# Optimization experiments

Measured on AMD Instinct MI355X. Metric: run time of the kernel, lower is better.

Reference implementation:

```python
import jax, jax.numpy as jnp
import numpy as np

N_LAYERS = 2
D_MODEL = 768
D_INNER = 1536
D_STATE = 16
D_CONV = 4
DT_RANK = 48
VOCAB = 50257
EPS = 1e-5


def _rms(x, w):
    return x * jax.lax.rsqrt(jnp.mean(x * x, axis=-1, keepdims=True) + EPS) * w


def _mixer(x, in_w, cw, cb, xp_w, dt_w, dt_b, a_log, d_skip, out_w):
    b, l, _ = x.shape
    xz = x @ in_w.T                                  # (b,l,2*d_in)
    u, z = jnp.split(xz, 2, axis=-1)                 # each (b,l,d_in)
    # causal depthwise conv1d
    uc = jax.lax.conv_general_dilated(
        u.transpose(0, 2, 1), cw[:, None, :], (1,), [(D_CONV - 1, 0)],
        feature_group_count=D_INNER, dimension_numbers=("NCH", "OIH", "NCH"))
    u = jax.nn.silu((uc + cb[:, None]).transpose(0, 2, 1))
    x_dbl = u @ xp_w.T                               # (b,l,dt_rank+2n)
    dt, B, C = jnp.split(x_dbl, [DT_RANK, DT_RANK + D_STATE], axis=-1)
    delta = jax.nn.softplus(dt @ dt_w.T + dt_b)      # (b,l,d_in)
    A = -jnp.exp(a_log)                              # (d_in,n)
    dA = jnp.exp(delta[..., None] * A)               # (b,l,d_in,n)
    dBu = delta[..., None] * B[:, :, None, :] * u[..., None]

    def step(h, inp):
        dA_t, dBu_t, C_t = inp
        h = dA_t * h + dBu_t
        return h, jnp.einsum("bdn,bn->bd", h, C_t)

    h0 = jnp.zeros((b, D_INNER, D_STATE), x.dtype)
    _, ys = jax.lax.scan(step, h0, (dA.transpose(1, 0, 2, 3),
                                    dBu.transpose(1, 0, 2, 3),
                                    C.transpose(1, 0, 2)))
    y = ys.transpose(1, 0, 2) + u * d_skip           # (b,l,d_in)
    y = y * jax.nn.silu(z)
    return y @ out_w.T


def setup_inputs() -> dict:
    key = jax.random.key(0)
    ks = jax.random.split(key, 12)
    std = 0.02
    emb = jax.random.normal(ks[0], (VOCAB, D_MODEL), jnp.float32) * std
    emb = emb.at[0].set(0.0)  # padding_idx=0
    tokens = jax.random.randint(ks[1], (2, 1024), 0, VOCAB)
    a_log = jnp.tile(jnp.log(jnp.arange(1, D_STATE + 1, dtype=jnp.float32)),
                     (N_LAYERS, D_INNER, 1))
    return {
        "tokens": tokens,
        "emb": emb,
        "norm_w": jnp.ones((N_LAYERS, D_MODEL), jnp.float32),
        "in_proj_w": jax.random.normal(ks[2], (N_LAYERS, 2 * D_INNER, D_MODEL), jnp.float32) * std,
        "conv_w": jax.random.normal(ks[3], (N_LAYERS, D_INNER, D_CONV), jnp.float32) * 0.1,
        "conv_b": jnp.zeros((N_LAYERS, D_INNER), jnp.float32),
        "x_proj_w": jax.random.normal(ks[4], (N_LAYERS, DT_RANK + 2 * D_STATE, D_INNER), jnp.float32) * std,
        "dt_proj_w": jax.random.normal(ks[5], (N_LAYERS, D_INNER, DT_RANK), jnp.float32) * (DT_RANK ** -0.5),
        "dt_proj_b": jax.random.uniform(ks[6], (N_LAYERS, D_INNER), jnp.float32, -4.6, -2.0),
        "A_log": a_log,
        "D": jnp.ones((N_LAYERS, D_INNER), jnp.float32),
        "out_proj_w": jax.random.normal(ks[7], (N_LAYERS, D_MODEL, D_INNER), jnp.float32) * (std / np.sqrt(2 * N_LAYERS)),
        "normf_w": jnp.ones((D_MODEL,), jnp.float32),
        "lm_head_w": jax.random.normal(ks[8], (VOCAB, D_MODEL), jnp.float32) * std,
    }


def reference(tokens, emb, norm_w, in_proj_w, conv_w, conv_b, x_proj_w,
              dt_proj_w, dt_proj_b, A_log, D, out_proj_w, normf_w, lm_head_w):
    x = emb[tokens]                                  # (b,l,d_model)
    for i in range(N_LAYERS):
        x = x + _mixer(_rms(x, norm_w[i]), in_proj_w[i], conv_w[i], conv_b[i],
                       x_proj_w[i], dt_proj_w[i], dt_proj_b[i], A_log[i],
                       D[i], out_proj_w[i])
    x = _rms(x, normf_w)
    return x @ lm_head_w.T                           # (b,l,vocab)
```

## Files before the change

kernel.cpp:

```cpp
#include <hip/hip_runtime.h>
#include <hip/hip_bf16.h>
#include <math.h>

#define DM 768
#define DI 1536
#define DSN 16
#define NB 2
#define SL 1024
#define MROWS 2048
#define VOC 50257
#define VOCP 50432
#define EPSR 1e-5f

typedef __attribute__((ext_vector_type(8))) short short8;
typedef __attribute__((ext_vector_type(4))) float f32x4;
typedef __attribute__((ext_vector_type(4))) unsigned short us4;
typedef unsigned short u16;

__device__ inline u16 f2bf(float f) {
    unsigned u = __builtin_bit_cast(unsigned, f);
    u += 0x7FFFu + ((u >> 16) & 1u);
    return (u16)(u >> 16);
}

#define G_LDS16(g, l) __builtin_amdgcn_global_load_lds( \
    (const __attribute__((address_space(1))) void*)(g), \
    (__attribute__((address_space(3))) void*)(l), 16, 0, 0)

__global__ __launch_bounds__(256)
void k_embed_rms(const int* __restrict__ tok, const float* __restrict__ emb,
                 const float* __restrict__ w, float* __restrict__ x,
                 u16* __restrict__ out) {
    int r = blockIdx.x;
    int t = tok[r];
    const float* src = emb + (size_t)t * DM;
    int c0 = threadIdx.x * 3;
    float v[3]; float ss = 0.f;
#pragma unroll
    for (int i = 0; i < 3; ++i) {
        v[i] = src[c0 + i]; ss += v[i] * v[i];
        x[(size_t)r * DM + c0 + i] = v[i];
    }
#pragma unroll
    for (int o = 32; o > 0; o >>= 1) ss += __shfl_down(ss, o);
    __shared__ float s[4];
    int lane = threadIdx.x & 63, wv = threadIdx.x >> 6;
    if (lane == 0) s[wv] = ss;
    __syncthreads();
    float sc = rsqrtf((s[0] + s[1] + s[2] + s[3]) / (float)DM + EPSR);
#pragma unroll
    for (int i = 0; i < 3; ++i)
        out[(size_t)r * DM + c0 + i] = f2bf(v[i] * sc * w[c0 + i]);
}

__global__ __launch_bounds__(256)
void k_rmsnorm_bf16(const float* __restrict__ x, const float* __restrict__ w,
                    u16* __restrict__ out) {
    int r = blockIdx.x;
    const float* row = x + (size_t)r * DM;
    int c0 = threadIdx.x * 3;
    float v[3]; float ss = 0.f;
#pragma unroll
    for (int i = 0; i < 3; ++i) { v[i] = row[c0 + i]; ss += v[i] * v[i]; }
#pragma unroll
    for (int o = 32; o > 0; o >>= 1) ss += __shfl_down(ss, o);
    __shared__ float s[4];
    int lane = threadIdx.x & 63, wv = threadIdx.x >> 6;
    if (lane == 0) s[wv] = ss;
    __syncthreads();
    float sc = rsqrtf((s[0] + s[1] + s[2] + s[3]) / (float)DM + EPSR);
#pragma unroll
    for (int i = 0; i < 3; ++i)
        out[(size_t)r * DM + c0 + i] = f2bf(v[i] * sc * w[c0 + i]);
}

struct CvtSeg { const float* src; u16* dst; int sr, sc, sld, dc, blk0, total4; };
struct CvtArgs { CvtSeg seg[9]; };

__global__ __launch_bounds__(256)
void k_cvt_multi(CvtArgs a) {
    int b = blockIdx.x;
    int s = 0;
#pragma unroll
    for (int q = 1; q < 9; ++q) if (a.seg[q].blk0 <= b) s = q;
    const CvtSeg& g = a.seg[s];
    long i4 = (long)(b - g.blk0) * 256 + threadIdx.x;
    if (i4 >= g.total4) return;
    long i = i4 * 4;
    int r = (int)(i / g.dc), c0 = (int)(i % g.dc);
    us4 o;
#pragma unroll
    for (int e = 0; e < 4; ++e) {
        int c = c0 + e;
        float v = (r < g.sr && c < g.sc) ? g.src[(size_t)r * g.sld + c] : 0.f;
        o[e] = f2bf(v);
    }
    *(us4*)&g.dst[i] = o;
}

__global__ void k_conv_silu(const float* __restrict__ xz, const float* __restrict__ cw,
                            const float* __restrict__ cb, float* __restrict__ uc,
                            u16* __restrict__ ucb) {
    int d = blockIdx.x * 256 + threadIdx.x;
    int r = blockIdx.y;
    int l = r & (SL - 1);
    float acc = cb[d];
#pragma unroll
    for (int j = 0; j < 4; ++j) {
        int ls = l - 3 + j;
        if (ls >= 0) acc += xz[(size_t)(r - 3 + j) * (2 * DI) + d] * cw[d * 4 + j];
    }
    float s = acc / (1.f + __expf(-acc));
    uc[(size_t)r * DI + d] = s;
    ucb[(size_t)r * DI + d] = f2bf(s);
}

__global__ __launch_bounds__(256)
void k_xp_red(const float* __restrict__ part, float* __restrict__ xdbl,
              u16* __restrict__ xdblb) {
    int idx = blockIdx.x * 256 + threadIdx.x;
    int row = idx >> 7, col = idx & 127;
    const float* p = part + (size_t)row * 1024 + col;
    float s = 0.f;
#pragma unroll
    for (int k = 0; k < 8; ++k) s += p[k * 128];
    xdbl[(size_t)row * 128 + col] = s;
    if (col < 64) xdblb[(size_t)row * 64 + col] = f2bf(s);
}

__global__ __launch_bounds__(512)
void k_scan2(const float* __restrict__ delta, const float* __restrict__ uc,
             const float* __restrict__ xdbl, const float* __restrict__ xz,
             const float* __restrict__ alog, const float* __restrict__ Dp,
             u16* __restrict__ ybf) {
    __shared__ float ds2[8][16][20], us2[8][16][20], bn2[8][16][20], cn2[8][16][20];
    __shared__ float Sm[8][16][16], Pm[8][16][16];
    int b  = blockIdx.x / 96;
    int d0 = (blockIdx.x % 96) * 16;
    int tid = threadIdx.x, w = tid >> 6, lane = tid & 63;
    int ch = lane >> 2, nq = lane & 3;
    int d = d0 + ch;
    float A[4];
#pragma unroll
    for (int k = 0; k < 4; ++k) A[k] = -__expf(alog[d * DSN + nq + 4 * k]);
    int tb = w * 128;

    float h[4] = {0.f, 0.f, 0.f, 0.f};
    float sdl = 0.f;
    for (int t0 = 0; t0 < 128; t0 += 16) {
        int row0 = b * SL + tb + t0;
#pragma unroll
        for (int i = 0; i < 4; ++i) {
            int lin = i * 64 + lane, tt = lin >> 4, cc = lin & 15;
            size_t row = (size_t)(row0 + tt);
            ds2[w][cc][tt] = delta[row * DI + d0 + cc];
            us2[w][cc][tt] = uc[row * DI + d0 + cc];
            bn2[w][cc][tt] = xdbl[row * 128 + 48 + cc];
        }
#pragma unroll
        for (int g4 = 0; g4 < 4; ++g4) {
            f32x4 dl = *(const f32x4*)&ds2[w][ch][g4 * 4];
            f32x4 uv = *(const f32x4*)&us2[w][ch][g4 * 4];
            f32x4 bv[4];
#pragma unroll
            for (int k = 0; k < 4; ++k) bv[k] = *(const f32x4*)&bn2[w][nq + 4 * k][g4 * 4];
#pragma unroll
            for (int s = 0; s < 4; ++s) {
                float du = dl[s] * uv[s];
                sdl += dl[s];
#pragma unroll
                for (int k = 0; k < 4; ++k) {
                    float dA = __expf(dl[s] * A[k]);
                    h[k] = h[k] * dA + du * bv[k][s];
                }
            }
        }
    }
#pragma unroll
    for (int k = 0; k < 4; ++k) {
        Sm[w][ch][nq + 4 * k] = h[k];
        Pm[w][ch][nq + 4 * k] = __expf(A[k] * sdl);
    }
    __syncthreads();
    if (tid < 256) {
        int c2 = tid >> 4, n2 = tid & 15;
        float H = 0.f;
#pragma unroll
        for (int g = 0; g < 8; ++g) {
            float hi = H;
            H = Pm[g][c2][n2] * H + Sm[g][c2][n2];
            Sm[g][c2][n2] = hi;
        }
    }
    __syncthreads();
    float Dv = Dp[d];
#pragma unroll
    for (int k = 0; k < 4; ++k) h[k] = Sm[w][ch][nq + 4 * k];
    for (int t0 = 0; t0 < 128; t0 += 16) {
        int row0 = b * SL + tb + t0;
#pragma unroll
        for (int i = 0; i < 4; ++i) {
            int lin = i * 64 + lane, tt = lin >> 4, cc = lin & 15;
            size_t row = (size_t)(row0 + tt);
            ds2[w][cc][tt] = delta[row * DI + d0 + cc];
            us2[w][cc][tt] = uc[row * DI + d0 + cc];
            bn2[w][cc][tt] = xdbl[row * 128 + 48 + cc];
            cn2[w][cc][tt] = xdbl[row * 128 + 64 + cc];
        }
#pragma unroll
        for (int g4 = 0; g4 < 4; ++g4) {
            f32x4 dl = *(const f32x4*)&ds2[w][ch][g4 * 4];
            f32x4 uv = *(const f32x4*)&us2[w][ch][g4 * 4];
            f32x4 bv[4], cv[4];
#pragma unroll
            for (int k = 0; k < 4; ++k) {
                bv[k] = *(const f32x4*)&bn2[w][nq + 4 * k][g4 * 4];
                cv[k] = *(const f32x4*)&cn2[w][nq + 4 * k][g4 * 4];
            }
#pragma unroll
            for (int s = 0; s < 4; ++s) {
                float du = dl[s] * uv[s];
                float p = 0.f;
#pragma unroll
                for (int k = 0; k < 4; ++k) {
                    float dA = __expf(dl[s] * A[k]);
                    h[k] = h[k] * dA + du * bv[k][s];
                    p += h[k] * cv[k][s];
                }
                p += __shfl_xor(p, 1);
                p += __shfl_xor(p, 2);
                if (nq == 0) {
                    size_t row = (size_t)(row0 + g4 * 4 + s);
                    float z = xz[row * (2 * DI) + DI + d];
                    float y = p + uv[s] * Dv;
                    y *= z / (1.f + __expf(-z));
                    ybf[row * DI + d] = f2bf(y);
                }
            }
        }
    }
}

template <int EPIL, bool SPLITK>
__global__ __launch_bounds__(256)
void k_gemm_bt(const u16* __restrict__ A, const u16* __restrict__ W,
               float* C, const float* RES,
               const float* __restrict__ BIASV,
               int K, int ldk, int ldc, int nTm) {
    __shared__ u16 Al[128 * 32];
    __shared__ u16 Wl[128 * 32];
    int nwg = gridDim.x;
    int qc = nwg >> 3, rc = nwg & 7;
    int xcd = blockIdx.x & 7, j = blockIdx.x >> 3;
    int wg = (xcd < rc ? xcd * (qc + 1) : rc * (qc + 1) + (xcd - rc) * qc) + j;
    int m0 = (wg % nTm) * 128;
    int sl = wg / nTm;
    int n0 = SPLITK ? 0 : sl * 128;
    int cb = SPLITK ? sl * 128 : n0;
    int kb = SPLITK ? sl * K : 0;

    int tid = threadIdx.x, wave = tid >> 6, lane = tid & 63;
    int wm = wave >> 1, wn = wave & 1;
    f32x4 acc[4][4] = {};
    const int rS = (lane >> 2);
    const int kS = (((lane & 3) ^ ((lane >> 3) & 3)) * 8);
    const int kofs = (((lane >> 4) ^ ((lane >> 1) & 3)) * 8);
    const int fr = lane & 15;

    for (int k0 = 0; k0 < K; k0 += 32) {
#pragma unroll
        for (int i = 0; i < 2; ++i) {
            int rowA = m0 + wave * 32 + i * 16 + rS;
            G_LDS16(A + (size_t)rowA * ldk + kb + k0 + kS, &Al[wave * 1024 + i * 512]);
            int rowW = n0 + wave * 32 + i * 16 + rS;
            G_LDS16(W + (size_t)rowW * ldk + kb + k0 + kS, &Wl[wave * 1024 + i * 512]);
        }
        __syncthreads();
        short8 af[4], bfr[4];
#pragma unroll
        for (int f = 0; f < 4; ++f) {
            af[f]  = *(const short8*)&Al[(wm * 64 + f * 16 + fr) * 32 + kofs];
            bfr[f] = *(const short8*)&Wl[(wn * 64 + f * 16 + fr) * 32 + kofs];
        }
#pragma unroll
        for (int i = 0; i < 4; ++i)
#pragma unroll
            for (int jj = 0; jj < 4; ++jj)
                acc[i][jj] = __builtin_amdgcn_mfma_f32_16x16x32_bf16(af[i], bfr[jj], acc[i][jj], 0, 0, 0);
        __syncthreads();
    }
    int r4 = (lane >> 4) * 4;
#pragma unroll
    for (int i = 0; i < 4; ++i)
#pragma unroll
        for (int jj = 0; jj < 4; ++jj) {
            int col = cb + wn * 64 + jj * 16 + fr;
            float bia = (EPIL == 2) ? BIASV[col] : 0.f;
#pragma unroll
            for (int rr = 0; rr < 4; ++rr) {
                int row = m0 + wm * 64 + i * 16 + r4 + rr;
                size_t off = (size_t)row * ldc + col;
                float v = acc[i][jj][rr];
                if (EPIL == 1) v += RES[off];
                if (EPIL == 2) { v += bia; v = (v > 20.f) ? v : log1pf(__expf(v)); }
                C[off] = v;
            }
        }
}

#define BAR  __builtin_amdgcn_s_barrier()
#define LGK0 do { asm volatile("s_waitcnt lgkmcnt(0)" ::: "memory"); \
                  __builtin_amdgcn_sched_barrier(0); } while (0)
#define VMC3 asm volatile("s_waitcnt vmcnt(3)" ::: "memory")
#define VMC0 asm volatile("s_waitcnt vmcnt(0)" ::: "memory")

#define STAGE1(t, op, half, GB, RB) do {                                      \
    const u16* _g = (GB) + (size_t)((RB) + (half) * 128 + (w << 4) + srow) * K \
                    + (t) * 32 + scol;                                         \
    G_LDS16(_g, &lds[(t) & 1][op][half][w << 9]);                              \
} while (0)

#define RDA(dst, t, mq) do {                                                   \
    _Pragma("unroll") for (int _m = 0; _m < 4; ++_m)                           \
        dst[_m] = *(const short8*)&lds[(t) & 1][0][wm]                         \
            [((mq) * 64 + _m * 16 + fr) * 32 + rd_sw];                         \
} while (0)

#define RDB(t, nq) do {                                                       \
    _Pragma("unroll") for (int _n = 0; _n < 2; ++_n)                           \
        bfv[_n] = *(const short8*)&lds[(t) & 1][1][wbh]                        \
            [(wbr * 64 + (nq) * 32 + _n * 16 + fr) * 32 + rd_sw];              \
} while (0)

#define MM8(AF, mq, nq) do {                                                  \
    __builtin_amdgcn_s_setprio(1);                                            \
    _Pragma("unroll") for (int _m = 0; _m < 4; ++_m)                           \
    _Pragma("unroll") for (int _n = 0; _n < 2; ++_n)                           \
        acc[(mq) * 4 + _m][(nq) * 2 + _n] =                                    \
            __builtin_amdgcn_mfma_f32_16x16x32_bf16(                           \
                AF[_m], bfv[_n], acc[(mq) * 4 + _m][(nq) * 2 + _n], 0, 0, 0);  \
    __builtin_amdgcn_s_setprio(0);                                            \
} while (0)

template <int K>
__global__ __launch_bounds__(512, 2)
void k_gemm256(const u16* __restrict__ Ap, const u16* __restrict__ Wp,
               float* __restrict__ C, int ldc, int nmax, int nTm) {
    constexpr int NT = K / 32;
    constexpr int NI = NT / 2;
    __shared__ __align__(16) u16 lds[2][2][2][4096];

    int per8 = gridDim.x >> 3;
    int wg = (blockIdx.x & 7) * per8 + (blockIdx.x >> 3);
    int m0 = (wg % nTm) * 256, n0 = (wg / nTm) * 256;

    int tid = threadIdx.x, w = tid >> 6, lane = tid & 63;
    int wm = w >> 2, wn = w & 3, wbh = wn >> 1, wbr = wn & 1;
    int fr = lane & 15;
    int rd_sw = (((lane >> 4) ^ ((lane >> 1) & 3)) * 8);
    int srow  = lane >> 2;
    int scol  = (((lane & 3) ^ ((lane >> 3) & 3)) * 8);

    f32x4 acc[8][4] = {};
    short8 af0[4], af1[4], bfv[2];

    STAGE1(0, 0, 0, Ap, m0); STAGE1(0, 0, 1, Ap, m0);
    STAGE1(0, 1, 0, Wp, n0); STAGE1(0, 1, 1, Wp, n0);
    STAGE1(1, 0, 0, Ap, m0); STAGE1(1, 0, 1, Ap, m0);
    STAGE1(1, 1, 0, Wp, n0);
    VMC3; BAR;

    for (int i = 0; i < NI - 1; ++i) {
        const int ta = 2 * i, tb = 2 * i + 1;
        RDA(af0, ta, 0); RDA(af1, ta, 1); RDB(ta, 0);
        STAGE1(tb, 1, 1, Wp, n0);
        STAGE1(ta + 2, 0, 0, Ap, m0);
        BAR; LGK0; MM8(af0, 0, 0); MM8(af1, 1, 0); BAR;
        RDB(ta, 1);
        STAGE1(ta + 2, 0, 1, Ap, m0);
        STAGE1(ta + 2, 1, 0, Wp, n0);
        BAR; LGK0; MM8(af1, 1, 1); MM8(af0, 0, 1); VMC3; BAR;
        RDA(af0, tb, 0); RDA(af1, tb, 1); RDB(tb, 0);
        STAGE1(ta + 2, 1, 1, Wp, n0);
        STAGE1(ta + 3, 0, 0, Ap, m0);
        BAR; LGK0; MM8(af0, 0, 0); MM8(af1, 1, 0); BAR;
        RDB(tb, 1);
        STAGE1(ta + 3, 0, 1, Ap, m0);
        STAGE1(ta + 3, 1, 0, Wp, n0);
        BAR; LGK0; MM8(af1, 1, 1); MM8(af0, 0, 1); VMC3; BAR;
    }
    {
        const int ta = NT - 2, tb = NT - 1;
        RDA(af0, ta, 0); RDA(af1, ta, 1); RDB(ta, 0);
        STAGE1(tb, 1, 1, Wp, n0);
        BAR; LGK0; MM8(af0, 0, 0); MM8(af1, 1, 0); BAR;
        RDB(ta, 1);
        BAR; LGK0; MM8(af1, 1, 1); MM8(af0, 0, 1); VMC0; BAR;
        RDA(af0, tb, 0); RDA(af1, tb, 1); RDB(tb, 0);
        BAR; LGK0; MM8(af0, 0, 0); MM8(af1, 1, 0); BAR;
        RDB(tb, 1);
        BAR; LGK0; MM8(af1, 1, 1); MM8(af0, 0, 1); BAR;
    }

    int r4 = (lane >> 4) * 4;
#pragma unroll
    for (int mi = 0; mi < 8; ++mi)
#pragma unroll
        for (int ni = 0; ni < 4; ++ni) {
            int col = n0 + wn * 64 + (ni >> 1) * 32 + (ni & 1) * 16 + fr;
            if (col >= nmax) continue;
            int row = m0 + wm * 128 + (mi >> 2) * 64 + (mi & 3) * 16 + r4;
#pragma unroll
            for (int rr = 0; rr < 4; ++rr)
                C[(size_t)(row + rr) * ldc + col] = acc[mi][ni][rr];
        }
}

extern "C" void kernel_launch(void* const* d_in, const int* in_sizes, int n_in,
                              void* d_out, int out_size, void* d_ws, size_t ws_size,
                              hipStream_t stream) {
    (void)in_sizes; (void)n_in; (void)out_size;
    const int*   tok   = (const int*)d_in[0];
    const float* emb   = (const float*)d_in[1];
    const float* normw = (const float*)d_in[2];
    const float* inw   = (const float*)d_in[3];
    const float* cw    = (const float*)d_in[4];
    const float* cb    = (const float*)d_in[5];
    const float* xpw   = (const float*)d_in[6];
    const float* dtw   = (const float*)d_in[7];
    const float* dtb   = (const float*)d_in[8];
    const float* alog  = (const float*)d_in[9];
    const float* Dp    = (const float*)d_in[10];
    const float* outw  = (const float*)d_in[11];
    const float* normf = (const float*)d_in[12];
    const float* lmw   = (const float*)d_in[13];
    float* out = (float*)d_out;

    char* p = (char*)d_ws;
    auto alloc = [&](size_t bytes) { char* r = p; p += (bytes + 255) & ~(size_t)255; return r; };
    float* x     = (float*)alloc((size_t)MROWS * DM * 4);
    u16*   xnb   = (u16*)  alloc((size_t)MROWS * DM * 2);
    float* xz    = (float*)alloc((size_t)MROWS * 2 * DI * 4);
    float* uc    = (float*)alloc((size_t)MROWS * DI * 4);
    u16*   ucb   = (u16*)  alloc((size_t)MROWS * DI * 2);
    float* xdbl  = (float*)alloc((size_t)MROWS * 128 * 4);
    u16*   xdblb = (u16*)  alloc((size_t)MROWS * 64 * 2);
    float* part  = (float*)alloc((size_t)MROWS * 1024 * 4);
    float* delta = (float*)alloc((size_t)MROWS * DI * 4);
    u16*   ybf   = (u16*)  alloc((size_t)MROWS * DI * 2);
    u16*   winb  = (u16*)  alloc((size_t)NB * (2 * DI) * DM * 2);
    u16*   wxpb  = (u16*)  alloc((size_t)NB * 128 * DI * 2);
    u16*   wdtb  = (u16*)  alloc((size_t)NB * DI * 64 * 2);
    u16*   woutb = (u16*)  alloc((size_t)NB * DM * DI * 2);
    u16*   wlmb  = (u16*)  alloc((size_t)VOCP * DM * 2);
    if ((size_t)(p - (char*)d_ws) > ws_size) return;

    CvtArgs ca;
    int blk = 0;
    auto seg = [&](int idx, const float* s, u16* d, int sr, int sc, int sld, int dc, int dr) {
        int t4 = dr * dc / 4;
        ca.seg[idx] = CvtSeg{s, d, sr, sc, sld, dc, blk, t4};
        blk += (t4 + 255) / 256;
    };
    seg(0, lmw, wlmb, VOC, DM, DM, DM, VOCP);
    seg(1, inw,                          winb,                          2 * DI, DM, DM, DM, 2 * DI);
    seg(2, inw + (size_t)2 * DI * DM,    winb + (size_t)2 * DI * DM,    2 * DI, DM, DM, DM, 2 * DI);
    seg(3, xpw,                          wxpb,                          80, DI, DI, DI, 128);
    seg(4, xpw + (size_t)80 * DI,        wxpb + (size_t)128 * DI,       80, DI, DI, DI, 128);
    seg(5, dtw,                          wdtb,                          DI, 48, 48, 64, DI);
    seg(6, dtw + (size_t)DI * 48,        wdtb + (size_t)DI * 64,        DI, 48, 48, 64, DI);
    seg(7, outw,                         woutb,                         DM, DI, DI, DI, DM);
    seg(8, outw + (size_t)DM * DI,       woutb + (size_t)DM * DI,       DM, DI, DI, DI, DM);
    k_cvt_multi<<<dim3(blk), 256, 0, stream>>>(ca);

    k_embed_rms<<<MROWS, 256, 0, stream>>>(tok, emb, normw, x, xnb);

    for (int i = 0; i < NB; ++i) {
        if (i > 0)
            k_rmsnorm_bf16<<<MROWS, 256, 0, stream>>>(x, normw + i * DM, xnb);

        k_gemm_bt<0, false><<<dim3(16 * (2 * DI / 128)), 256, 0, stream>>>(
            xnb, winb + (size_t)i * 2 * DI * DM, xz, nullptr, nullptr,
            DM, DM, 2 * DI, 16);

        k_conv_silu<<<dim3(DI / 256, MROWS), 256, 0, stream>>>(
            xz, cw + (size_t)i * DI * 4, cb + (size_t)i * DI, uc, ucb);

        k_gemm_bt<0, true><<<dim3(16 * 8), 256, 0, stream>>>(
            ucb, wxpb + (size_t)i * 128 * DI, part, nullptr, nullptr,
            DI / 8, DI, 1024, 16);
        k_xp_red<<<dim3(MROWS * 128 / 256), 256, 0, stream>>>(part, xdbl, xdblb);

        k_gemm_bt<2, false><<<dim3(16 * (DI / 128)), 256, 0, stream>>>(
            xdblb, wdtb + (size_t)i * DI * 64, delta, nullptr, dtb + (size_t)i * DI,
            64, 64, DI, 16);

        k_scan2<<<dim3(NB * (DI / 16)), 512, 0, stream>>>(
            delta, uc, xdbl, xz, alog + (size_t)i * DI * DSN, Dp + i * DI, ybf);

        k_gemm_bt<1, false><<<dim3(16 * (DM / 128)), 256, 0, stream>>>(
            ybf, woutb + (size_t)i * DM * DI, x, x, nullptr, DI, DI, DM, 16);
    }

    k_rmsnorm_bf16<<<MROWS, 256, 0, stream>>>(x, normf, xnb);
    k_gemm256<DM><<<dim3(8 * (VOCP / 256)), 512, 0, stream>>>(
        xnb, wlmb, out, VOC, VOC, 8);
}
```

Before: 747.7 us.

## Triple-buffer LDS staging in the 256x256 bf16 GEMM main loop

Replaces the double-buffered LDS pipeline of the 256x256 MFMA GEMM with a three-buffer rotation. Each k-tile now prefetches the A and B halves of tile t+2 while computing tile t, which gives global loads a full extra tile of latency slack and simplifies the schedule into a uniform TILE macro. The cost is that LDS per block grows from 64KB to 96KB. With launch bounds asking for two 512-thread blocks per CU, that may no longer fit, which could halve occupancy. K must now be a multiple of 96.

```diff
diff --git a/kernel.cpp b/kernel.cpp
--- a/kernel.cpp
+++ b/kernel.cpp
@@ -311,24 +311,24 @@
 #define BAR  __builtin_amdgcn_s_barrier()
 #define LGK0 do { asm volatile("s_waitcnt lgkmcnt(0)" ::: "memory"); \
                   __builtin_amdgcn_sched_barrier(0); } while (0)
-#define VMC3 asm volatile("s_waitcnt vmcnt(3)" ::: "memory")
+#define VMC4 asm volatile("s_waitcnt vmcnt(4)" ::: "memory")
 #define VMC0 asm volatile("s_waitcnt vmcnt(0)" ::: "memory")
 
-#define STAGE1(t, op, half, GB, RB) do {                                      \
+#define STG(t, b, op, half, GB, RB) do {                                       \
     const u16* _g = (GB) + (size_t)((RB) + (half) * 128 + (w << 4) + srow) * K \
                     + (t) * 32 + scol;                                         \
-    G_LDS16(_g, &lds[(t) & 1][op][half][w << 9]);                              \
+    G_LDS16(_g, &lds[b][op][half][w << 9]);                                    \
 } while (0)
 
-#define RDA(dst, t, mq) do {                                                   \
+#define RDA(dst, b, mq) do {                                                   \
     _Pragma("unroll") for (int _m = 0; _m < 4; ++_m)                           \
-        dst[_m] = *(const short8*)&lds[(t) & 1][0][wm]                         \
+        dst[_m] = *(const short8*)&lds[b][0][wm]                               \
             [((mq) * 64 + _m * 16 + fr) * 32 + rd_sw];                         \
 } while (0)
 
-#define RDB(t, nq) do {                                                       \
+#define RDB(b, nq) do {                                                       \
     _Pragma("unroll") for (int _n = 0; _n < 2; ++_n)                           \
-        bfv[_n] = *(const short8*)&lds[(t) & 1][1][wbh]                        \
+        bfv[_n] = *(const short8*)&lds[b][1][wbh]                              \
             [(wbr * 64 + (nq) * 32 + _n * 16 + fr) * 32 + rd_sw];              \
 } while (0)
 
@@ -342,13 +342,28 @@
     __builtin_amdgcn_s_setprio(0);                                            \
 } while (0)
 
+#define TILE(t, bR, bS, STAGE_ON, WAIT) do {                                   \
+                                                                       \
+    RDA(af0, bR, 0); RDA(af1, bR, 1); RDB(bR, 0);                              \
+    if (STAGE_ON) { STG((t) + 2, bS, 0, 0, Ap, m0);                            \
+                    STG((t) + 2, bS, 0, 1, Ap, m0); }                          \
+    BAR; LGK0; MM8(af0, 0, 0); MM8(af1, 1, 0); BAR;                            \
+                                                                       \
+    RDB(bR, 1);                                                                \
+    if (STAGE_ON) { STG((t) + 2, bS, 1, 0, Wp, n0);                            \
+                    STG((t) + 2, bS, 1, 1, Wp, n0); }                          \
+    BAR; LGK0; MM8(af1, 1, 1); MM8(af0, 0, 1);                                 \
+    if ((WAIT) == 0) { VMC4; } else if ((WAIT) == 1) { VMC0; }                 \
+    BAR;                                                                       \
+} while (0)
+
 template <int K>
 __global__ __launch_bounds__(512, 2)
 void k_gemm256(const u16* __restrict__ Ap, const u16* __restrict__ Wp,
                float* __restrict__ C, int ldc, int nmax, int nTm) {
     constexpr int NT = K / 32;
-    constexpr int NI = NT / 2;
-    __shared__ __align__(16) u16 lds[2][2][2][4096];
+    static_assert(NT % 3 == 0 && NT >= 6, "NT must be a multiple of 3");
+    __shared__ __align__(16) u16 lds[3][2][2][4096];
 
     int per8 = gridDim.x >> 3;
     int wg = (blockIdx.x & 7) * per8 + (blockIdx.x >> 3);
@@ -364,43 +379,21 @@
     f32x4 acc[8][4] = {};
     short8 af0[4], af1[4], bfv[2];
 
-    STAGE1(0, 0, 0, Ap, m0); STAGE1(0, 0, 1, Ap, m0);
-    STAGE1(0, 1, 0, Wp, n0); STAGE1(0, 1, 1, Wp, n0);
-    STAGE1(1, 0, 0, Ap, m0); STAGE1(1, 0, 1, Ap, m0);
-    STAGE1(1, 1, 0, Wp, n0);
-    VMC3; BAR;
-
-    for (int i = 0; i < NI - 1; ++i) {
-        const int ta = 2 * i, tb = 2 * i + 1;
-        RDA(af0, ta, 0); RDA(af1, ta, 1); RDB(ta, 0);
-        STAGE1(tb, 1, 1, Wp, n0);
-        STAGE1(ta + 2, 0, 0, Ap, m0);
-        BAR; LGK0; MM8(af0, 0, 0); MM8(af1, 1, 0); BAR;
-        RDB(ta, 1);
-        STAGE1(ta + 2, 0, 1, Ap, m0);
-        STAGE1(ta + 2, 1, 0, Wp, n0);
-        BAR; LGK0; MM8(af1, 1, 1); MM8(af0, 0, 1); VMC3; BAR;
-        RDA(af0, tb, 0); RDA(af1, tb, 1); RDB(tb, 0);
-        STAGE1(ta + 2, 1, 1, Wp, n0);
-        STAGE1(ta + 3, 0, 0, Ap, m0);
-        BAR; LGK0; MM8(af0, 0, 0); MM8(af1, 1, 0); BAR;
-        RDB(tb, 1);
-        STAGE1(ta + 3, 0, 1, Ap, m0);
-        STAGE1(ta + 3, 1, 0, Wp, n0);
-        BAR; LGK0; MM8(af1, 1, 1); MM8(af0, 0, 1); VMC3; BAR;
-    }
-    {
-        const int ta = NT - 2, tb = NT - 1;
-        RDA(af0, ta, 0); RDA(af1, ta, 1); RDB(ta, 0);
-        STAGE1(tb, 1, 1, Wp, n0);
-        BAR; LGK0; MM8(af0, 0, 0); MM8(af1, 1, 0); BAR;
-        RDB(ta, 1);
-        BAR; LGK0; MM8(af1, 1, 1); MM8(af0, 0, 1); VMC0; BAR;
-        RDA(af0, tb, 0); RDA(af1, tb, 1); RDB(tb, 0);
-        BAR; LGK0; MM8(af0, 0, 0); MM8(af1, 1, 0); BAR;
-        RDB(tb, 1);
-        BAR; LGK0; MM8(af1, 1, 1); MM8(af0, 0, 1); BAR;
-    }
+    STG(0, 0, 0, 0, Ap, m0); STG(0, 0, 0, 1, Ap, m0);
+    STG(0, 0, 1, 0, Wp, n0); STG(0, 0, 1, 1, Wp, n0);
+    STG(1, 1, 0, 0, Ap, m0); STG(1, 1, 0, 1, Ap, m0);
+    STG(1, 1, 1, 0, Wp, n0); STG(1, 1, 1, 1, Wp, n0);
+    VMC4; BAR;
+
+    for (int j = 0; j < NT / 3 - 1; ++j) {
+        const int t0 = 3 * j;
+        TILE(t0,     0, 2, 1, 0);
+        TILE(t0 + 1, 1, 0, 1, 0);
+        TILE(t0 + 2, 2, 1, 1, 0);
+    }
+    TILE(NT - 3, 0, 2, 1, 0);
+    TILE(NT - 2, 1, 0, 0, 1);
+    TILE(NT - 1, 2, 0, 0, 2);
 
     int r4 = (lane >> 4) * 4;
 #pragma unroll
```

Result: no change. 737.9 us (-1.3%).
